# Kernel tuning notes

Hardware: AMD Instinct MI355X
Metric: run time of the kernel (lower is better)

The kernel has to match this reference:

```python
import jax, jax.numpy as jnp
import numpy as np

D_MODEL = 512
NUM_HEADS = 8
WINDOW = 64
HEAD_DIM = D_MODEL // NUM_HEADS


def setup_inputs() -> dict:
    key = jax.random.key(0)
    k1, k2, k3 = jax.random.split(key, 3)
    B, F, L, D = 4, 16, 2048, D_MODEL
    x = jax.random.normal(k1, (B, F, L, D), dtype=jnp.float32)
    w_qkv = jax.random.normal(k2, (D, 3 * D), dtype=jnp.float32) * (1.0 / np.sqrt(D))
    b_qkv = jnp.zeros((3 * D,), dtype=jnp.float32)
    w_proj = jax.random.normal(k3, (D, D), dtype=jnp.float32) * (1.0 / np.sqrt(D))
    b_proj = jnp.zeros((D,), dtype=jnp.float32)
    return {"x": x, "w_qkv": w_qkv, "b_qkv": b_qkv, "w_proj": w_proj, "b_proj": b_proj}


def reference(x, w_qkv, b_qkv, w_proj, b_proj):
    B, F, L, D = x.shape
    W = WINDOW
    H, hd = NUM_HEADS, HEAD_DIM
    nw = L // W  # L chosen divisible by window_size; pad path is identity here
    # partition into windows: (B, F, nw, W, D)
    xw = x.reshape(B, F, nw, W, D)
    # fused QKV projection
    qkv = jnp.einsum('bfnwd,de->bfnwe', xw, w_qkv) + b_qkv  # (B,F,nw,W,3D)
    qkv = qkv.reshape(B, F, nw, W, 3, H, hd)
    q = qkv[..., 0, :, :]  # (B,F,nw,W,H,hd)
    k = qkv[..., 1, :, :]
    v = qkv[..., 2, :, :]
    scale = 1.0 / np.sqrt(hd).astype(np.float32)
    # per-window attention: scores (B,F,nw,H,W,W)
    scores = jnp.einsum('bfnqhd,bfnkhd->bfnhqk', q, k) * scale
    attn = jax.nn.softmax(scores, axis=-1)
    out = jnp.einsum('bfnhqk,bfnkhd->bfnqhd', attn, v)  # (B,F,nw,W,H,hd)
    out = out.reshape(B, F, nw, W, D)
    out = jnp.einsum('bfnwd,de->bfnwe', out, w_proj) + b_proj
    return out.reshape(B, F, L, D)
```

## Files before the change

kernel.cpp:

```cpp
#include <hip/hip_runtime.h>

typedef __attribute__((ext_vector_type(8))) short short8;
typedef __attribute__((ext_vector_type(4))) float f32x4;
typedef unsigned short u16;
typedef unsigned int u32;

__device__ __forceinline__ u16 f2bf(float f){
  union { float f; u32 u; } v; v.f = f;
  u32 u = v.u;
  u32 r = (u + 0x7FFFu + ((u >> 16) & 1u)) >> 16;
  return (u16)r;
}

__device__ __forceinline__ u32 cvtpk(float a, float b){
  u32 r;
  asm("v_cvt_pk_bf16_f32 %0, %1, %2" : "=v"(r) : "v"(a), "v"(b));
  return r;
}

__device__ __forceinline__ int swz(int row, int cb){ return cb ^ ((row & 7) << 4); }

__device__ __forceinline__ void gload16(const void* g, void* l){
  __builtin_amdgcn_global_load_lds(
      (const __attribute__((address_space(1))) unsigned int*)g,
      (__attribute__((address_space(3))) unsigned int*)l, 16, 0, 0);
}

__global__ void convert_weights_swz(const float* __restrict__ wqkv,
                                    const float* __restrict__ wproj,
                                    u16* __restrict__ wq_swz,
                                    u16* __restrict__ wpt){
  int c = blockIdx.x * 256 + threadIdx.x;
  union { u16 u[8]; uint4 v; } t;
  if (c < 98304){
    int tile = c >> 10, row = (c >> 3) & 127, c7 = c & 7;
    int bn = tile >> 3, kt = tile & 7;
    int j  = c7 ^ (row & 7);
    int e  = bn * 128 + row;
    int k0 = kt * 64 + j * 8;
    #pragma unroll
    for (int i = 0; i < 8; ++i) t.u[i] = f2bf(wqkv[(long)(k0 + i) * 1536 + e]);
    *reinterpret_cast<uint4*>(wq_swz + (long)c * 8) = t.v;
  } else {
    int t2 = c - 98304;
    int cc = t2 >> 6;
    int kc = (t2 & 63) << 3;
    #pragma unroll
    for (int i = 0; i < 8; ++i) t.u[i] = f2bf(wproj[(long)(kc + i) * 512 + cc]);
    *reinterpret_cast<uint4*>(wpt + (long)cc * 512 + kc) = t.v;
  }
}

__global__ void convert_x(const float* __restrict__ x, u16* __restrict__ xbf){
  int c = blockIdx.x * 256 + threadIdx.x;
  int tile = c >> 10, row = (c >> 3) & 127, c7 = c & 7;
  int bm = tile >> 3, kt = tile & 7;
  int j  = c7 ^ (row & 7);
  const float* src = x + (long)(bm * 128 + row) * 512 + kt * 64 + j * 8;
  float4 v0 = *reinterpret_cast<const float4*>(src);
  float4 v1 = *reinterpret_cast<const float4*>(src + 4);
  union { u16 u[8]; uint4 v; } t;
  t.u[0] = f2bf(v0.x); t.u[1] = f2bf(v0.y); t.u[2] = f2bf(v0.z); t.u[3] = f2bf(v0.w);
  t.u[4] = f2bf(v1.x); t.u[5] = f2bf(v1.y); t.u[6] = f2bf(v1.z); t.u[7] = f2bf(v1.w);
  *reinterpret_cast<uint4*>(xbf + (long)c * 8) = t.v;
}

__global__ __launch_bounds__(512, 2) void qkv_gemm256(
    const u16*  __restrict__ xbf,
    const u16*  __restrict__ wswz,
    const float* __restrict__ bqkv,
    u16* __restrict__ qkv)
{
  __shared__ char smem[131072];

  const int tid = threadIdx.x;
  const int l = tid & 63, w = tid >> 6;
  const int g = l >> 4,  ln = l & 15;
  const int wm = w >> 2, wn = w & 3;

  int hb   = blockIdx.x;
  int work = (hb & 7) * 384 + (hb >> 3);
  int bn   = work % 6;
  int bm   = work / 6;

  f32x4 acc[8][4];
  #pragma unroll
  for (int m = 0; m < 8; ++m)
    #pragma unroll
    for (int n = 0; n < 4; ++n) acc[m][n] = (f32x4){0.f,0.f,0.f,0.f};

  auto stage_part = [&](int d, int kt, int p){
    const char* src; char* dst;
    if (p == 0){
      src = (const char*)xbf  + ((long)(bm*2+0)*8 + kt)*16384;
      dst = smem + d*32768;
    } else if (p == 1){
      src = (const char*)xbf  + ((long)(bm*2+1)*8 + kt)*16384;
      dst = smem + d*32768 + 16384;
    } else if (p == 2){
      src = (const char*)wswz + ((long)(bn*2+0)*8 + kt)*16384;
      dst = smem + 65536 + d*32768;
    } else {
      src = (const char*)wswz + ((long)(bn*2+1)*8 + kt)*16384;
      dst = smem + 65536 + d*32768 + 16384;
    }
    gload16(src + (long)tid*16,         dst + w*1024);
    gload16(src + (long)(512+tid)*16,   dst + 8192 + w*1024);
  };

  #pragma unroll
  for (int p = 0; p < 4; ++p) stage_part(0, 0, p);
  asm volatile("s_waitcnt vmcnt(0)");
  __syncthreads();

  const int brow0 = (wn & 1) * 64;
  for (int t = 0; t < 8; ++t){
    const int cur = t & 1;
    const char* Abase = smem + cur*32768 + wm*16384;
    const char* Bbase = smem + 65536 + cur*32768 + (wn >> 1)*16384;
    #pragma unroll
    for (int p = 0; p < 4; ++p){
      if (t < 7) stage_part(cur^1, t+1, p);
      const int mh = p >> 1, nh = p & 1;
      short8 a[4][2], b[2][2];
      #pragma unroll
      for (int i = 0; i < 4; ++i){
        int rowl = (mh*4 + i)*16 + ln;
        #pragma unroll
        for (int ks = 0; ks < 2; ++ks)
          a[i][ks] = *reinterpret_cast<const short8*>(
              Abase + rowl*128 + (((ks*4 + g) ^ (rowl & 7)) << 4));
      }
      #pragma unroll
      for (int j = 0; j < 2; ++j){
        int rowl = brow0 + (nh*2 + j)*16 + ln;
        #pragma unroll
        for (int ks = 0; ks < 2; ++ks)
          b[j][ks] = *reinterpret_cast<const short8*>(
              Bbase + rowl*128 + (((ks*4 + g) ^ (rowl & 7)) << 4));
      }
      __builtin_amdgcn_s_setprio(1);
      #pragma unroll
      for (int i = 0; i < 4; ++i)
        #pragma unroll
        for (int j = 0; j < 2; ++j)
          #pragma unroll
          for (int ks = 0; ks < 2; ++ks)
            acc[mh*4+i][nh*2+j] = __builtin_amdgcn_mfma_f32_16x16x32_bf16(
                a[i][ks], b[j][ks], acc[mh*4+i][nh*2+j], 0, 0, 0);
      __builtin_amdgcn_s_setprio(0);
    }
    asm volatile("s_waitcnt vmcnt(0)" ::: "memory");
    __syncthreads();
  }

  u16* ldsC = (u16*)smem;
  #pragma unroll
  for (int ph = 0; ph < 2; ++ph){
    #pragma unroll
    for (int mf = 0; mf < 4; ++mf){
      int m = ph*4 + mf;
      #pragma unroll
      for (int n = 0; n < 4; ++n){
        int col = wn*64 + n*16 + ln;
        float bias = bqkv[bn*256 + col];
        int lr0 = wm*64 + mf*16 + g*4;
        #pragma unroll
        for (int r = 0; r < 4; ++r)
          ldsC[(lr0 + r)*264 + col] = f2bf(acc[m][n][r] + bias);
      }
    }
    __syncthreads();
    {
      int lr = tid >> 2, seg = tid & 3;
      const char* src = (const char*)(ldsC + lr*264) + seg*128;
      long gr = (long)bm*256 + (lr >> 6)*128 + ph*64 + (lr & 63);
      char* dst = (char*)qkv + (gr*1536 + bn*256)*2 + seg*128;
      #pragma unroll
      for (int j = 0; j < 8; ++j)
        *reinterpret_cast<uint4*>(dst + j*16) = *reinterpret_cast<const uint4*>(src + j*16);
    }
    __syncthreads();
  }
}

__global__ __launch_bounds__(512, 4) void winattn_proj(
    const u16* __restrict__ qkv,
    const u16* __restrict__ wpt,
    const float* __restrict__ bproj,
    float* __restrict__ out)
{
  __shared__ u16 lds[8][4096];
  const int tid = threadIdx.x;
  const int l = tid & 63, w = tid >> 6;
  const int g = l >> 4,  ln = l & 15;
  const int gh = g >> 1, gl = g & 1;
  const long tokb = (long)blockIdx.x * 64;
  u16* vt = lds[w];
  const int h = w;

  {
    const int dg = l & 3, tg = l >> 2;
    uint4 vr[4][2];
    #pragma unroll
    for (int r = 0; r < 4; ++r){
      const char* vrow = (const char*)(qkv + (tokb + tg*4 + r) * 1536 + 1024 + h*64 + dg*16);
      vr[r][0] = *reinterpret_cast<const uint4*>(vrow);
      vr[r][1] = *reinterpret_cast<const uint4*>(vrow + 16);
    }
    #pragma unroll
    for (int dd = 0; dd < 16; ++dd){
      int d = dg*16 + dd;
      int sub = dd & 7, hi = dd >> 3;
      uint2 pk;
      pk.x = (u32)((const u16*)&vr[0][hi])[sub] | ((u32)((const u16*)&vr[1][hi])[sub] << 16);
      pk.y = (u32)((const u16*)&vr[2][hi])[sub] | ((u32)((const u16*)&vr[3][hi])[sub] << 16);
      *reinterpret_cast<uint2*>((char*)vt + d*128 + swz(d, tg*8)) = pk;
    }
  }

  f32x4 oacc[4][4];
  #pragma unroll
  for (int m = 0; m < 4; ++m)
    #pragma unroll
    for (int n = 0; n < 4; ++n) oacc[m][n] = (f32x4){0.f,0.f,0.f,0.f};

  const int lnA = ln + 32*gl;

  #pragma unroll
  for (int half = 0; half < 2; ++half){
    short8 qa[2][2];
    #pragma unroll
    for (int j = 0; j < 2; ++j){
      const char* qrow = (const char*)(qkv + (tokb + (half*2+j)*16 + ln) * 1536 + h*64 + g*8);
      qa[j][0] = *reinterpret_cast<const short8*>(qrow);
      qa[j][1] = *reinterpret_cast<const short8*>(qrow + 64);
    }
    f32x4 st[4][2];
    #pragma unroll
    for (int mk = 0; mk < 4; ++mk){
      st[mk][0] = (f32x4){0.f,0.f,0.f,0.f};
      st[mk][1] = (f32x4){0.f,0.f,0.f,0.f};
    }
    #pragma unroll
    for (int mk = 0; mk < 4; ++mk){
      const char* krow = (const char*)(qkv + (tokb + mk*16 + ln) * 1536 + 512 + h*64 + g*8);
      short8 kb0 = *reinterpret_cast<const short8*>(krow);
      short8 kb1 = *reinterpret_cast<const short8*>(krow + 64);
      #pragma unroll
      for (int j = 0; j < 2; ++j){
        st[mk][j] = __builtin_amdgcn_mfma_f32_16x16x32_bf16(kb0, qa[j][0], st[mk][j], 0, 0, 0);
        st[mk][j] = __builtin_amdgcn_mfma_f32_16x16x32_bf16(kb1, qa[j][1], st[mk][j], 0, 0, 0);
      }
    }
    u32 warr[4][2][2];
    #pragma unroll
    for (int j = 0; j < 2; ++j){
      float mx = -3.4e38f;
      #pragma unroll
      for (int mk = 0; mk < 4; ++mk)
        #pragma unroll
        for (int r = 0; r < 4; ++r) mx = fmaxf(mx, st[mk][j][r]);
      mx = fmaxf(mx, __shfl_xor(mx, 16, 64));
      mx = fmaxf(mx, __shfl_xor(mx, 32, 64));
      float s = 0.f;
      #pragma unroll
      for (int mk = 0; mk < 4; ++mk)
        #pragma unroll
        for (int r = 0; r < 4; ++r){
          float p = __expf((st[mk][j][r] - mx) * 0.125f);
          st[mk][j][r] = p; s += p;
        }
      s += __shfl_xor(s, 16, 64);
      s += __shfl_xor(s, 32, 64);
      float inv = 1.f / s;
      #pragma unroll
      for (int mk = 0; mk < 4; ++mk){
        warr[mk][j][0] = cvtpk(st[mk][j][0]*inv, st[mk][j][1]*inv);
        warr[mk][j][1] = cvtpk(st[mk][j][2]*inv, st[mk][j][3]*inv);
      }
    }
    __builtin_amdgcn_s_setprio(1);
    #pragma unroll
    for (int ks = 0; ks < 2; ++ks){
      short8 vb[4];
      #pragma unroll
      for (int n = 0; n < 4; ++n){
        int row = n*16 + ln;
        vb[n] = *reinterpret_cast<const short8*>((char*)vt + row*128 + swz(row, (ks*32 + g*8)*2));
      }
      #pragma unroll
      for (int mo = 0; mo < 2; ++mo){
        int m = half*2 + mo;
        u32 c0a = warr[2*ks  ][mo][0], c0b = warr[2*ks  ][mo][1];
        u32 c1a = warr[2*ks+1][mo][0], c1b = warr[2*ks+1][mo][1];
        u32 s0a = (u32)__shfl((int)c0a, lnA, 64);
        u32 s1a = (u32)__shfl((int)c1a, lnA, 64);
        u32 s0b = (u32)__shfl((int)c0b, lnA, 64);
        u32 s1b = (u32)__shfl((int)c1b, lnA, 64);
        u32 t0a = (u32)__shfl((int)c0a, lnA+16, 64);
        u32 t1a = (u32)__shfl((int)c1a, lnA+16, 64);
        u32 t0b = (u32)__shfl((int)c0b, lnA+16, 64);
        u32 t1b = (u32)__shfl((int)c1b, lnA+16, 64);
        union { u32 u[4]; short8 v; } pf;
        pf.u[0] = gh ? s1a : s0a;
        pf.u[1] = gh ? s1b : s0b;
        pf.u[2] = gh ? t1a : t0a;
        pf.u[3] = gh ? t1b : t0b;
        #pragma unroll
        for (int n = 0; n < 4; ++n)
          oacc[m][n] = __builtin_amdgcn_mfma_f32_16x16x32_bf16(pf.v, vb[n], oacc[m][n], 0, 0, 0);
      }
    }
    __builtin_amdgcn_s_setprio(0);
  }

  #pragma unroll
  for (int m = 0; m < 4; ++m)
    #pragma unroll
    for (int n = 0; n < 4; ++n){
      int d = n*16 + ln;
      #pragma unroll
      for (int r = 0; r < 4; ++r){
        int t = m*16 + g*4 + r;
        *reinterpret_cast<u16*>((char*)vt + t*128 + swz(t, d*2)) = f2bf(oacc[m][n][r]);
      }
    }

  __syncthreads();

  f32x4 acc[4][4];
  #pragma unroll
  for (int m = 0; m < 4; ++m)
    #pragma unroll
    for (int n = 0; n < 4; ++n) acc[m][n] = (f32x4){0.f,0.f,0.f,0.f};

  for (int hh = 0; hh < 8; ++hh){
    const char* obuf = (const char*)lds[hh];
    #pragma unroll
    for (int ks = 0; ks < 2; ++ks){
      short8 a[4], b[4];
      #pragma unroll
      for (int m = 0; m < 4; ++m){
        int row = m*16 + ln;
        a[m] = *reinterpret_cast<const short8*>(obuf + row*128 + swz(row, (ks*32 + g*8)*2));
      }
      #pragma unroll
      for (int n = 0; n < 4; ++n){
        int e = w*64 + n*16 + ln;
        b[n] = *reinterpret_cast<const short8*>(wpt + (long)e*512 + hh*64 + ks*32 + g*8);
      }
      __builtin_amdgcn_s_setprio(1);
      #pragma unroll
      for (int m = 0; m < 4; ++m)
        #pragma unroll
        for (int n = 0; n < 4; ++n)
          acc[m][n] = __builtin_amdgcn_mfma_f32_16x16x32_bf16(a[m], b[n], acc[m][n], 0, 0, 0);
      __builtin_amdgcn_s_setprio(0);
    }
  }

  #pragma unroll
  for (int n = 0; n < 4; ++n){
    int col = w*64 + n*16 + ln;
    float bias = bproj[col];
    #pragma unroll
    for (int m = 0; m < 4; ++m){
      #pragma unroll
      for (int r = 0; r < 4; ++r){
        int t = m*16 + g*4 + r;
        out[(tokb + t) * 512 + col] = acc[m][n][r] + bias;
      }
    }
  }
}

__global__ void convert_weights(const float* __restrict__ wqkv,
                                const float* __restrict__ wproj,
                                u16* __restrict__ wqkvt,
                                u16* __restrict__ wprojt){
  int tid = blockIdx.x * 256 + threadIdx.x;
  union { u16 u[8]; uint4 v; } tmp;
  if (tid < 1536 * 64){
    int e  = tid >> 6;
    int kc = (tid & 63) << 3;
    #pragma unroll
    for (int i = 0; i < 8; ++i) tmp.u[i] = f2bf(wqkv[(long)(kc + i) * 1536 + e]);
    *reinterpret_cast<uint4*>(wqkvt + (long)e * 512 + kc) = tmp.v;
  } else {
    int t2 = tid - 1536 * 64;
    int c  = t2 >> 6;
    int kc = (t2 & 63) << 3;
    #pragma unroll
    for (int i = 0; i < 8; ++i) tmp.u[i] = f2bf(wproj[(long)(kc + i) * 512 + c]);
    *reinterpret_cast<uint4*>(wprojt + (long)c * 512 + kc) = tmp.v;
  }
}

__global__ __launch_bounds__(512, 2) void fused_winattn(
    const float* __restrict__ x,
    const u16*  __restrict__ wqkvt,
    const float* __restrict__ bqkv,
    const u16*  __restrict__ wprojt,
    const float* __restrict__ bproj,
    float* __restrict__ out)
{
  __shared__ u16 lds_x[64 * 512];
  __shared__ u16 lds_q[64 * 64];
  __shared__ u16 lds_k[64 * 64];
  __shared__ u16 lds_vt[64 * 64];
  __shared__ u16 lds_p[64 * 64];

  const int tid = threadIdx.x;
  const int l   = tid & 63;
  const int w   = tid >> 6;
  const int g   = l >> 4;
  const int ln  = l & 15;
  const long tokbase = (long)blockIdx.x * 64;

  {
    const float4* xv = reinterpret_cast<const float4*>(x + tokbase * 512);
    #pragma unroll
    for (int j = 0; j < 16; ++j){
      int i   = j * 512 + tid;
      int row = i >> 7;
      int c4  = i & 127;
      float4 v = xv[i];
      uint2 pk;
      pk.x = (u32)f2bf(v.x) | ((u32)f2bf(v.y) << 16);
      pk.y = (u32)f2bf(v.z) | ((u32)f2bf(v.w) << 16);
      int byte = row * 1024 + swz(row, c4 * 8);
      *reinterpret_cast<uint2*>(reinterpret_cast<char*>(lds_x) + byte) = pk;
    }
  }

  f32x4 oacc[4][4];
  #pragma unroll
  for (int m = 0; m < 4; ++m)
    #pragma unroll
    for (int n = 0; n < 4; ++n) oacc[m][n] = (f32x4){0.f, 0.f, 0.f, 0.f};

  const int mw   = w & 3;
  const int half = w >> 2;

  __syncthreads();

  for (int h = 0; h < 8; ++h){
    f32x4 qacc[6];
    #pragma unroll
    for (int j = 0; j < 6; ++j) qacc[j] = (f32x4){0.f, 0.f, 0.f, 0.f};
    int ebase[6];
    #pragma unroll
    for (int j = 0; j < 6; ++j){
      int nt = half * 6 + j;
      int sec = nt >> 2;
      ebase[j] = sec * 512 + h * 64 + (nt & 3) * 16;
    }
    const int arow = mw * 16 + ln;
    #pragma unroll
    for (int ks = 0; ks < 16; ++ks){
      short8 a = *reinterpret_cast<const short8*>(
          reinterpret_cast<const char*>(lds_x) + arow * 1024 + swz(arow, (ks * 32 + g * 8) * 2));
      #pragma unroll
      for (int j = 0; j < 6; ++j){
        short8 b = *reinterpret_cast<const short8*>(
            wqkvt + (long)(ebase[j] + ln) * 512 + ks * 32 + g * 8);
        qacc[j] = __builtin_amdgcn_mfma_f32_16x16x32_bf16(a, b, qacc[j], 0, 0, 0);
      }
    }
    #pragma unroll
    for (int j = 0; j < 6; ++j){
      int nt  = half * 6 + j;
      int sec = nt >> 2;
      float bias = bqkv[ebase[j] + ln];
      if (sec < 2){
        u16* dst = (sec == 0) ? lds_q : lds_k;
        int c = (nt & 3) * 16 + ln;
        #pragma unroll
        for (int r = 0; r < 4; ++r){
          int t = mw * 16 + g * 4 + r;
          int byte = t * 128 + swz(t, c * 2);
          *reinterpret_cast<u16*>(reinterpret_cast<char*>(dst) + byte) = f2bf(qacc[j][r] + bias);
        }
      } else {
        int d  = (nt & 3) * 16 + ln;
        int t0 = mw * 16 + g * 4;
        uint2 pk;
        pk.x = (u32)f2bf(qacc[j][0] + bias) | ((u32)f2bf(qacc[j][1] + bias) << 16);
        pk.y = (u32)f2bf(qacc[j][2] + bias) | ((u32)f2bf(qacc[j][3] + bias) << 16);
        int byte = d * 128 + swz(d, t0 * 2);
        *reinterpret_cast<uint2*>(reinterpret_cast<char*>(lds_vt) + byte) = pk;
      }
    }
    __syncthreads();

    if (w < 4){
      f32x4 sacc[4];
      #pragma unroll
      for (int jt = 0; jt < 4; ++jt) sacc[jt] = (f32x4){0.f, 0.f, 0.f, 0.f};
      #pragma unroll
      for (int ks = 0; ks < 2; ++ks){
        int qrow = w * 16 + ln;
        short8 a = *reinterpret_cast<const short8*>(
            reinterpret_cast<const char*>(lds_q) + qrow * 128 + swz(qrow, (ks * 32 + g * 8) * 2));
        #pragma unroll
        for (int jt = 0; jt < 4; ++jt){
          int krow = jt * 16 + ln;
          short8 b = *reinterpret_cast<const short8*>(
              reinterpret_cast<const char*>(lds_k) + krow * 128 + swz(krow, (ks * 32 + g * 8) * 2));
          sacc[jt] = __builtin_amdgcn_mfma_f32_16x16x32_bf16(a, b, sacc[jt], 0, 0, 0);
        }
      }
      #pragma unroll
      for (int r = 0; r < 4; ++r){
        float mx = fmaxf(fmaxf(sacc[0][r], sacc[1][r]), fmaxf(sacc[2][r], sacc[3][r]));
        mx = fmaxf(mx, __shfl_xor(mx, 1, 64));
        mx = fmaxf(mx, __shfl_xor(mx, 2, 64));
        mx = fmaxf(mx, __shfl_xor(mx, 4, 64));
        mx = fmaxf(mx, __shfl_xor(mx, 8, 64));
        float p[4], s = 0.f;
        #pragma unroll
        for (int jt = 0; jt < 4; ++jt){
          p[jt] = __expf((sacc[jt][r] - mx) * 0.125f);
          s += p[jt];
        }
        s += __shfl_xor(s, 1, 64);
        s += __shfl_xor(s, 2, 64);
        s += __shfl_xor(s, 4, 64);
        s += __shfl_xor(s, 8, 64);
        float inv = 1.f / s;
        int i = w * 16 + g * 4 + r;
        #pragma unroll
        for (int jt = 0; jt < 4; ++jt){
          int c = jt * 16 + ln;
          int byte = i * 128 + swz(i, c * 2);
          *reinterpret_cast<u16*>(reinterpret_cast<char*>(lds_p) + byte) = f2bf(p[jt] * inv);
        }
      }
    }
    __syncthreads();

    {
      int mc  = w & 3;
      int nc0 = (w >> 2) * 2;
      f32x4 oc[2];
      oc[0] = (f32x4){0.f, 0.f, 0.f, 0.f};
      oc[1] = (f32x4){0.f, 0.f, 0.f, 0.f};
      #pragma unroll
      for (int ks = 0; ks < 2; ++ks){
        int prow = mc * 16 + ln;
        short8 a = *reinterpret_cast<const short8*>(
            reinterpret_cast<const char*>(lds_p) + prow * 128 + swz(prow, (ks * 32 + g * 8) * 2));
        #pragma unroll
        for (int jj = 0; jj < 2; ++jj){
          int vrow = (nc0 + jj) * 16 + ln;
          short8 b = *reinterpret_cast<const short8*>(
              reinterpret_cast<const char*>(lds_vt) + vrow * 128 + swz(vrow, (ks * 32 + g * 8) * 2));
          oc[jj] = __builtin_amdgcn_mfma_f32_16x16x32_bf16(a, b, oc[jj], 0, 0, 0);
        }
      }
      #pragma unroll
      for (int jj = 0; jj < 2; ++jj){
        int d = (nc0 + jj) * 16 + ln;
        #pragma unroll
        for (int r = 0; r < 4; ++r){
          int t = mc * 16 + g * 4 + r;
          int byte = t * 128 + swz(t, d * 2);
          *reinterpret_cast<u16*>(reinterpret_cast<char*>(lds_q) + byte) = f2bf(oc[jj][r]);
        }
      }
    }
    __syncthreads();

    #pragma unroll
    for (int ks = 0; ks < 2; ++ks){
      short8 a[4];
      #pragma unroll
      for (int m = 0; m < 4; ++m){
        int row = m * 16 + ln;
        a[m] = *reinterpret_cast<const short8*>(
            reinterpret_cast<const char*>(lds_q) + row * 128 + swz(row, (ks * 32 + g * 8) * 2));
      }
      #pragma unroll
      for (int nt = 0; nt < 4; ++nt){
        int e = w * 64 + nt * 16 + ln;
        short8 b = *reinterpret_cast<const short8*>(
            wprojt + (long)e * 512 + h * 64 + ks * 32 + g * 8);
        #pragma unroll
        for (int m = 0; m < 4; ++m)
          oacc[m][nt] = __builtin_amdgcn_mfma_f32_16x16x32_bf16(a[m], b, oacc[m][nt], 0, 0, 0);
      }
    }
    __syncthreads();
  }

  #pragma unroll
  for (int nt = 0; nt < 4; ++nt){
    int col = w * 64 + nt * 16 + ln;
    float bias = bproj[col];
    #pragma unroll
    for (int m = 0; m < 4; ++m){
      #pragma unroll
      for (int r = 0; r < 4; ++r){
        int t = m * 16 + g * 4 + r;
        out[(tokbase + t) * 512 + col] = oacc[m][nt][r] + bias;
      }
    }
  }
}

extern "C" void kernel_launch(void* const* d_in, const int* in_sizes, int n_in,
                              void* d_out, int out_size, void* d_ws, size_t ws_size,
                              hipStream_t stream) {
  const float* x     = (const float*)d_in[0];
  const float* wqkv  = (const float*)d_in[1];
  const float* bqkv  = (const float*)d_in[2];
  const float* wproj = (const float*)d_in[3];
  const float* bproj = (const float*)d_in[4];
  float* out = (float*)d_out;

  const size_t NEED = 538968064ULL;
  if (ws_size >= NEED){
    u16* wq_swz = (u16*)d_ws;
    u16* wpt    = (u16*)((char*)d_ws + 1572864);
    u16* xbf    = (u16*)((char*)d_ws + 2097152);
    u16* qkv    = (u16*)((char*)d_ws + 136314880);
    convert_weights_swz<<<512, 256, 0, stream>>>(wqkv, wproj, wq_swz, wpt);
    convert_x<<<32768, 256, 0, stream>>>(x, xbf);
    qkv_gemm256<<<3072, 512, 0, stream>>>(xbf, wq_swz, bqkv, qkv);
    winattn_proj<<<2048, 512, 0, stream>>>(qkv, wpt, bproj, out);
  } else {
    u16* wqkvt  = (u16*)d_ws;
    u16* wprojt = wqkvt + 1536 * 512;
    convert_weights<<<512, 256, 0, stream>>>(wqkv, wproj, wqkvt, wprojt);
    fused_winattn<<<2048, 512, 0, stream>>>(x, wqkvt, bqkv, wprojt, bproj, out);
  }
}
```

Before: 667.2 us.

## Restructure QKV GEMM main loop into four-slot LDS ring with deeper prefetch

Replaces the double-buffered A/B staging with a four-slot LDS ring where each slot holds matching halves of the A and B tiles. Loads now run up to two k-steps ahead, and the full-drain vmcnt(0) wait is replaced by a partial vmcnt(8) wait. Each k-step loads all of its A/B fragments into registers at once, then syncs with an LDS barrier, issues the next loads, and runs all MFMAs. The aim is to hide global-load latency behind compute and cut per-iteration sync stalls, at the cost of more registers and trickier correctness of the barrier and counter logic.

Measured after the change: 663.8 us. No clear change (-0.5%).

```diff
diff --git a/kernel.cpp b/kernel.cpp
--- a/kernel.cpp
+++ b/kernel.cpp
@@ -89,69 +89,58 @@
     #pragma unroll
     for (int n = 0; n < 4; ++n) acc[m][n] = (f32x4){0.f,0.f,0.f,0.f};
 
-  auto stage_part = [&](int d, int kt, int p){
-    const char* src; char* dst;
-    if (p == 0){
-      src = (const char*)xbf  + ((long)(bm*2+0)*8 + kt)*16384;
-      dst = smem + d*32768;
-    } else if (p == 1){
-      src = (const char*)xbf  + ((long)(bm*2+1)*8 + kt)*16384;
-      dst = smem + d*32768 + 16384;
-    } else if (p == 2){
-      src = (const char*)wswz + ((long)(bn*2+0)*8 + kt)*16384;
-      dst = smem + 65536 + d*32768;
-    } else {
-      src = (const char*)wswz + ((long)(bn*2+1)*8 + kt)*16384;
-      dst = smem + 65536 + d*32768 + 16384;
-    }
-    gload16(src + (long)tid*16,         dst + w*1024);
-    gload16(src + (long)(512+tid)*16,   dst + 8192 + w*1024);
+  auto stage_slot = [&](int s){
+    int kt = s >> 1, h = s & 1;
+    char* base = smem + (s & 3) * 32768;
+    const char* sa = (const char*)xbf  + ((long)(bm*2+h)*8 + kt)*16384;
+    const char* sb = (const char*)wswz + ((long)(bn*2+h)*8 + kt)*16384;
+    gload16(sa + (long)tid*16,         base + w*1024);
+    gload16(sa + (long)(512+tid)*16,   base + 8192 + w*1024);
+    gload16(sb + (long)tid*16,         base + 16384 + w*1024);
+    gload16(sb + (long)(512+tid)*16,   base + 24576 + w*1024);
   };
 
-  #pragma unroll
-  for (int p = 0; p < 4; ++p) stage_part(0, 0, p);
-  asm volatile("s_waitcnt vmcnt(0)");
-  __syncthreads();
-
-  const int brow0 = (wn & 1) * 64;
+  stage_slot(0); stage_slot(1); stage_slot(2); stage_slot(3);
+  asm volatile("s_waitcnt vmcnt(8)" ::: "memory");
+  __builtin_amdgcn_s_barrier();
+
+  const int bro = (wn & 1) * 64;
   for (int t = 0; t < 8; ++t){
-    const int cur = t & 1;
-    const char* Abase = smem + cur*32768 + wm*16384;
-    const char* Bbase = smem + 65536 + cur*32768 + (wn >> 1)*16384;
-    #pragma unroll
-    for (int p = 0; p < 4; ++p){
-      if (t < 7) stage_part(cur^1, t+1, p);
-      const int mh = p >> 1, nh = p & 1;
-      short8 a[4][2], b[2][2];
-      #pragma unroll
-      for (int i = 0; i < 4; ++i){
-        int rowl = (mh*4 + i)*16 + ln;
+    const char* Abase = smem + ((2*t + wm) & 3) * 32768;
+    const char* Bbase = smem + ((2*t + (wn >> 1)) & 3) * 32768 + 16384;
+    short8 a[8][2], b[4][2];
+    #pragma unroll
+    for (int m = 0; m < 8; ++m){
+      int r = m*16 + ln;
+      #pragma unroll
+      for (int ks = 0; ks < 2; ++ks)
+        a[m][ks] = *reinterpret_cast<const short8*>(
+            Abase + r*128 + (((ks*4 + g) ^ (r & 7)) << 4));
+    }
+    #pragma unroll
+    for (int n = 0; n < 4; ++n){
+      int r = bro + n*16 + ln;
+      #pragma unroll
+      for (int ks = 0; ks < 2; ++ks)
+        b[n][ks] = *reinterpret_cast<const short8*>(
+            Bbase + r*128 + (((ks*4 + g) ^ (r & 7)) << 4));
+    }
+    asm volatile("s_waitcnt lgkmcnt(0)" ::: "memory");
+    __builtin_amdgcn_s_barrier();
+    if (t < 6){ stage_slot(2*t + 4); stage_slot(2*t + 5); }
+    __builtin_amdgcn_s_setprio(1);
+    #pragma unroll
+    for (int m = 0; m < 8; ++m)
+      #pragma unroll
+      for (int n = 0; n < 4; ++n)
         #pragma unroll
         for (int ks = 0; ks < 2; ++ks)
-          a[i][ks] = *reinterpret_cast<const short8*>(
-              Abase + rowl*128 + (((ks*4 + g) ^ (rowl & 7)) << 4));
-      }
-      #pragma unroll
-      for (int j = 0; j < 2; ++j){
-        int rowl = brow0 + (nh*2 + j)*16 + ln;
-        #pragma unroll
-        for (int ks = 0; ks < 2; ++ks)
-          b[j][ks] = *reinterpret_cast<const short8*>(
-              Bbase + rowl*128 + (((ks*4 + g) ^ (rowl & 7)) << 4));
-      }
-      __builtin_amdgcn_s_setprio(1);
-      #pragma unroll
-      for (int i = 0; i < 4; ++i)
-        #pragma unroll
-        for (int j = 0; j < 2; ++j)
-          #pragma unroll
-          for (int ks = 0; ks < 2; ++ks)
-            acc[mh*4+i][nh*2+j] = __builtin_amdgcn_mfma_f32_16x16x32_bf16(
-                a[i][ks], b[j][ks], acc[mh*4+i][nh*2+j], 0, 0, 0);
-      __builtin_amdgcn_s_setprio(0);
-    }
-    asm volatile("s_waitcnt vmcnt(0)" ::: "memory");
-    __syncthreads();
+          acc[m][n] = __builtin_amdgcn_mfma_f32_16x16x32_bf16(
+              a[m][ks], b[n][ks], acc[m][n], 0, 0, 0);
+    __builtin_amdgcn_s_setprio(0);
+    if (t < 6)       asm volatile("s_waitcnt vmcnt(8)" ::: "memory");
+    else if (t == 6) asm volatile("s_waitcnt vmcnt(0)" ::: "memory");
+    if (t < 7) __builtin_amdgcn_s_barrier();
   }
 
   u16* ldsC = (u16*)smem;
```
